# Kernel optimization log

Hardware: AMD Instinct MI355X
Metric: run time of the kernel (lower is better)

## Reference

```python
import jax, jax.numpy as jnp
import numpy as np

T, D = 8192, 256   # frames, feature dim
P, K = 64, 128     # phone vocabulary, centers per phone


def setup_inputs() -> dict:
    key = jax.random.key(0)
    k1, k2, k3 = jax.random.split(key, 3)
    h = jax.random.normal(k1, (T, D), dtype=jnp.float32)
    centers = jax.random.normal(k2, (P, K, D), dtype=jnp.float32)
    phones = jax.random.randint(k3, (T,), 0, P, dtype=jnp.int64)
    return {"h": h, "centers": centers, "phones": phones}


def reference(h, centers, phones):
    """Per-phone 1-NN retrieval: for each frame t, find nearest center in the
    pool for phones[t] and return that center (anonymized feature).
    centers: [P, K, D] padded table replacing the (pattern, phone, gender) dict.
    """
    c = centers[phones]                                # [T, K, D] irregular gather
    # squared euclidean distance; ||h_t||^2 is constant per row -> omit for argmin
    d2 = jnp.sum(c * c, axis=-1) - 2.0 * jnp.einsum("td,tkd->tk", h, c)  # [T, K]
    idx = jnp.argmin(d2, axis=-1)                      # [T]
    h_anon = jnp.take_along_axis(c, idx[:, None, None], axis=1)[:, 0, :]  # [T, D]
    return h_anon
```

## Files before the change

### kernel.cpp

```cpp
#include <hip/hip_runtime.h>

#define T_FRAMES 8192
#define D_DIM    256
#define P_PHONES 64
#define K_CENT   128
#define TILE_F   16
#define MAX_TILES 576
#define MARGIN   1.0f

#define WS_NORMS  0
#define WS_FIDX   32768
#define WS_DESC   65536
#define WS_HH     131072
#define WS_CH     (131072 + 4194304)

typedef _Float16 half8 __attribute__((ext_vector_type(8)));
typedef float    f32x4 __attribute__((ext_vector_type(4)));

__global__ __launch_bounds__(1024) void qr_prep_kernel(const float* __restrict__ h,
                                                       const float* __restrict__ centers,
                                                       const int* __restrict__ phones,
                                                       float* __restrict__ norms,
                                                       int* __restrict__ fidx,
                                                       int4* __restrict__ desc,
                                                       _Float16* __restrict__ hH,
                                                       _Float16* __restrict__ cH) {
    const int b   = blockIdx.x;
    const int tid = threadIdx.x;

    if (b >= 513) {
        const int row  = (b - 513) * 16 + (tid >> 6);
        const int lane = tid & 63;
        const float4 cv = ((const float4*)(centers + (size_t)row * D_DIM))[lane];
        float s = cv.x * cv.x + cv.y * cv.y + cv.z * cv.z + cv.w * cv.w;
#pragma unroll
        for (int off = 32; off; off >>= 1) s += __shfl_xor(s, off, 64);
        if (lane == 0) norms[row] = s;
        return;
    }
    if (b >= 1) {
        const size_t e = ((size_t)(b - 1) * 1024 + tid) * 4;
        union { _Float16 hf[4]; uint2 u; } pk;
        float4 v = *(const float4*)(h + e);
        pk.hf[0] = (_Float16)v.x; pk.hf[1] = (_Float16)v.y;
        pk.hf[2] = (_Float16)v.z; pk.hf[3] = (_Float16)v.w;
        *(uint2*)(hH + e) = pk.u;
        v = *(const float4*)(centers + e);
        pk.hf[0] = (_Float16)v.x; pk.hf[1] = (_Float16)v.y;
        pk.hf[2] = (_Float16)v.z; pk.hf[3] = (_Float16)v.w;
        *(uint2*)(cH + e) = pk.u;
        return;
    }

    __shared__ int hist[P_PHONES];
    __shared__ int offp[P_PHONES];
    if (tid < P_PHONES) hist[tid] = 0;
    if (tid < 1024) desc[tid] = make_int4(0, 0, 0, 0);
    __syncthreads();
    for (int i = tid; i < T_FRAMES; i += 1024) atomicAdd(&hist[phones[i]], 1);
    __syncthreads();

    if (tid < 64) {
        const int c = hist[tid];
        int x = c;
#pragma unroll
        for (int off = 1; off < 64; off <<= 1) {
            int y = __shfl_up(x, off, 64);
            if (tid >= off) x += y;
        }
        const int fbase = x - c;
        offp[tid] = fbase;
        const int nt = (c + TILE_F - 1) / TILE_F;
        int tx = nt;
#pragma unroll
        for (int off = 1; off < 64; off <<= 1) {
            int y = __shfl_up(tx, off, 64);
            if (tid >= off) tx += y;
        }
        const int tb = tx - nt;
        for (int j = 0; j < nt; ++j)
            desc[tb + j] = make_int4(tid, fbase + j * TILE_F, min(TILE_F, c - j * TILE_F), 0);
    }
    __syncthreads();

    for (int i = tid; i < T_FRAMES; i += 1024) {
        const int p = phones[i];
        fidx[atomicAdd(&offp[p], 1)] = i;
    }
}

__global__ __launch_bounds__(256) void qr_main_kernel(const float* __restrict__ h,
                                                      const float* __restrict__ centers,
                                                      const float* __restrict__ norms,
                                                      const int* __restrict__ fidx,
                                                      const int4* __restrict__ desc,
                                                      const _Float16* __restrict__ hH,
                                                      const _Float16* __restrict__ cH,
                                                      float* __restrict__ out) {
    __shared__ float d2s[TILE_F * K_CENT];
    __shared__ float mins[TILE_F];
    __shared__ int   cnt[TILE_F];
    __shared__ short cand[TILE_F * 32];

    const int4 dsc = desc[blockIdx.x];
    const int fcnt = dsc.z;
    if (fcnt == 0) return;
    const int p = dsc.x, fstart = dsc.y;

    const int tid  = threadIdx.x;
    const int wave = tid >> 6;
    const int lane = tid & 63;
    const int m    = lane & 15;
    const int quad = lane >> 4;

    if (tid < TILE_F) cnt[tid] = 0;

    const int fiA = fidx[fstart + min(m, fcnt - 1)];
    const _Float16* ap = hH + (size_t)fiA * D_DIM + quad * 8;
    half8 aF[8];
#pragma unroll
    for (int s = 0; s < 8; ++s) aF[s] = *(const half8*)(ap + s * 32);

#pragma unroll
    for (int u = 0; u < 2; ++u) {
        const int c = (wave * 2 + u) * 16 + m;
        const _Float16* bp = cH + ((size_t)p * K_CENT + c) * D_DIM + quad * 8;
        f32x4 acc = {0.f, 0.f, 0.f, 0.f};
#pragma unroll
        for (int s = 0; s < 8; ++s)
            acc = __builtin_amdgcn_mfma_f32_16x16x32_f16(aF[s], *(const half8*)(bp + s * 32),
                                                         acc, 0, 0, 0);
        const float nrm = norms[p * K_CENT + c];
#pragma unroll
        for (int r = 0; r < 4; ++r)
            d2s[(quad * 4 + r) * K_CENT + c] = nrm - 2.0f * acc[r];
    }
    __syncthreads();

    {
        const int fr = tid >> 4;
        const int g  = tid & 15;
        float mn = 3.0e38f;
#pragma unroll
        for (int j = 0; j < 8; ++j) mn = fminf(mn, d2s[fr * K_CENT + g * 8 + j]);
#pragma unroll
        for (int off = 1; off < 16; off <<= 1) mn = fminf(mn, __shfl_xor(mn, off, 64));
        if (g == 0) mins[fr] = mn;
    }
    __syncthreads();

    {
        const int fr = tid >> 4;
        const int g  = tid & 15;
        const float tau = mins[fr] + MARGIN;
#pragma unroll
        for (int j = 0; j < 8; ++j) {
            const int c = g * 8 + j;
            if (d2s[fr * K_CENT + c] < tau) {
                const int pos = atomicAdd(&cnt[fr], 1);
                if (pos < 32) cand[fr * 32 + pos] = (short)c;
            }
        }
    }
    __syncthreads();

    for (int fr = wave; fr < fcnt; fr += 4) {
        const int fi = fidx[fstart + fr];
        const float4 hv = ((const float4*)(h + (size_t)fi * D_DIM))[lane];
        const int n = cnt[fr];
        float best = 3.0e38f; int bc = 0x7FFFFFFF;
        const int ncand = (n <= 32) ? n : K_CENT;
        for (int ci = 0; ci < ncand; ++ci) {
            const int c = (n <= 32) ? (int)cand[fr * 32 + ci] : ci;
            const float4 cv = ((const float4*)(centers + ((size_t)p * K_CENT + c) * D_DIM))[lane];
            float s = hv.x * cv.x + hv.y * cv.y + hv.z * cv.z + hv.w * cv.w;
#pragma unroll
            for (int off = 32; off; off >>= 1) s += __shfl_xor(s, off, 64);
            const float d2 = norms[p * K_CENT + c] - 2.0f * s;
            if (d2 < best || (d2 == best && c < bc)) { best = d2; bc = c; }
        }
        const float4 w4 = ((const float4*)(centers + ((size_t)p * K_CENT + bc) * D_DIM))[lane];
        ((float4*)(out + (size_t)fi * D_DIM))[lane] = w4;
    }
}

extern "C" void kernel_launch(void* const* d_in, const int* in_sizes, int n_in,
                              void* d_out, int out_size, void* d_ws, size_t ws_size,
                              hipStream_t stream) {
    const float* h       = (const float*)d_in[0];
    const float* centers = (const float*)d_in[1];
    const int*   phones  = (const int*)d_in[2];
    float*       out     = (float*)d_out;

    char* ws = (char*)d_ws;
    float*     norms = (float*)(ws + WS_NORMS);
    int*       fidx  = (int*)(ws + WS_FIDX);
    int4*      desc  = (int4*)(ws + WS_DESC);
    _Float16*  hH    = (_Float16*)(ws + WS_HH);
    _Float16*  cH    = (_Float16*)(ws + WS_CH);

    qr_prep_kernel<<<1025, 1024, 0, stream>>>(h, centers, phones, norms, fidx, desc, hH, cH);
    qr_main_kernel<<<MAX_TILES, 256, 0, stream>>>(h, centers, norms, fidx, desc, hH, cH, out);
}
```

Measured before the change: 91.12 us.

## Use 32-frame tiles, fuse norm computation into fp16 conversion, skip refine for unique candidates

```diff
diff --git a/kernel.cpp b/kernel.cpp
--- a/kernel.cpp
+++ b/kernel.cpp
@@ -4,8 +4,8 @@
 #define D_DIM    256
 #define P_PHONES 64
 #define K_CENT   128
-#define TILE_F   16
-#define MAX_TILES 576
+#define TILE_F   32
+#define MAX_TILES 320
 #define MARGIN   1.0f
 
 #define WS_NORMS  0
@@ -28,16 +28,6 @@
     const int b   = blockIdx.x;
     const int tid = threadIdx.x;
 
-    if (b >= 513) {
-        const int row  = (b - 513) * 16 + (tid >> 6);
-        const int lane = tid & 63;
-        const float4 cv = ((const float4*)(centers + (size_t)row * D_DIM))[lane];
-        float s = cv.x * cv.x + cv.y * cv.y + cv.z * cv.z + cv.w * cv.w;
-#pragma unroll
-        for (int off = 32; off; off >>= 1) s += __shfl_xor(s, off, 64);
-        if (lane == 0) norms[row] = s;
-        return;
-    }
     if (b >= 1) {
         const size_t e = ((size_t)(b - 1) * 1024 + tid) * 4;
         union { _Float16 hf[4]; uint2 u; } pk;
@@ -49,13 +39,17 @@
         pk.hf[0] = (_Float16)v.x; pk.hf[1] = (_Float16)v.y;
         pk.hf[2] = (_Float16)v.z; pk.hf[3] = (_Float16)v.w;
         *(uint2*)(cH + e) = pk.u;
+        float s = v.x * v.x + v.y * v.y + v.z * v.z + v.w * v.w;
+#pragma unroll
+        for (int off = 32; off; off >>= 1) s += __shfl_xor(s, off, 64);
+        if ((tid & 63) == 0) norms[(b - 1) * 16 + (tid >> 6)] = s;
         return;
     }
 
     __shared__ int hist[P_PHONES];
     __shared__ int offp[P_PHONES];
     if (tid < P_PHONES) hist[tid] = 0;
-    if (tid < 1024) desc[tid] = make_int4(0, 0, 0, 0);
+    if (tid < MAX_TILES) desc[tid] = make_int4(0, 0, 0, 0);
     __syncthreads();
     for (int i = tid; i < T_FRAMES; i += 1024) atomicAdd(&hist[phones[i]], 1);
     __syncthreads();
@@ -101,6 +95,9 @@
     __shared__ float mins[TILE_F];
     __shared__ int   cnt[TILE_F];
     __shared__ short cand[TILE_F * 32];
+    __shared__ int   widx[TILE_F];
+    __shared__ int   rlist[TILE_F];
+    __shared__ int   rn;
 
     const int4 dsc = desc[blockIdx.x];
     const int fcnt = dsc.z;
@@ -114,48 +111,58 @@
     const int quad = lane >> 4;
 
     if (tid < TILE_F) cnt[tid] = 0;
-
-    const int fiA = fidx[fstart + min(m, fcnt - 1)];
-    const _Float16* ap = hH + (size_t)fiA * D_DIM + quad * 8;
-    half8 aF[8];
-#pragma unroll
-    for (int s = 0; s < 8; ++s) aF[s] = *(const half8*)(ap + s * 32);
+    if (tid == 0) rn = 0;
+
+    half8 aF[2][8];
+#pragma unroll
+    for (int t = 0; t < 2; ++t) {
+        const int fiA = fidx[fstart + min(t * 16 + m, fcnt - 1)];
+        const _Float16* ap = hH + (size_t)fiA * D_DIM + quad * 8;
+#pragma unroll
+        for (int s = 0; s < 8; ++s) aF[t][s] = *(const half8*)(ap + s * 32);
+    }
 
 #pragma unroll
     for (int u = 0; u < 2; ++u) {
         const int c = (wave * 2 + u) * 16 + m;
         const _Float16* bp = cH + ((size_t)p * K_CENT + c) * D_DIM + quad * 8;
-        f32x4 acc = {0.f, 0.f, 0.f, 0.f};
-#pragma unroll
-        for (int s = 0; s < 8; ++s)
-            acc = __builtin_amdgcn_mfma_f32_16x16x32_f16(aF[s], *(const half8*)(bp + s * 32),
-                                                         acc, 0, 0, 0);
+        half8 bF[8];
+#pragma unroll
+        for (int s = 0; s < 8; ++s) bF[s] = *(const half8*)(bp + s * 32);
+        f32x4 acc0 = {0.f, 0.f, 0.f, 0.f};
+        f32x4 acc1 = {0.f, 0.f, 0.f, 0.f};
+#pragma unroll
+        for (int s = 0; s < 8; ++s) {
+            acc0 = __builtin_amdgcn_mfma_f32_16x16x32_f16(aF[0][s], bF[s], acc0, 0, 0, 0);
+            acc1 = __builtin_amdgcn_mfma_f32_16x16x32_f16(aF[1][s], bF[s], acc1, 0, 0, 0);
+        }
         const float nrm = norms[p * K_CENT + c];
 #pragma unroll
-        for (int r = 0; r < 4; ++r)
-            d2s[(quad * 4 + r) * K_CENT + c] = nrm - 2.0f * acc[r];
-    }
-    __syncthreads();
-
+        for (int r = 0; r < 4; ++r) {
+            d2s[(quad * 4 + r) * K_CENT + c]        = nrm - 2.0f * acc0[r];
+            d2s[(16 + quad * 4 + r) * K_CENT + c]   = nrm - 2.0f * acc1[r];
+        }
+    }
+    __syncthreads();
+
+    const int fr = tid >> 3;
+    const int g  = tid & 7;
     {
-        const int fr = tid >> 4;
-        const int g  = tid & 15;
         float mn = 3.0e38f;
 #pragma unroll
-        for (int j = 0; j < 8; ++j) mn = fminf(mn, d2s[fr * K_CENT + g * 8 + j]);
-#pragma unroll
-        for (int off = 1; off < 16; off <<= 1) mn = fminf(mn, __shfl_xor(mn, off, 64));
+        for (int j = 0; j < 16; ++j) mn = fminf(mn, d2s[fr * K_CENT + g * 16 + j]);
+        mn = fminf(mn, __shfl_xor(mn, 1, 64));
+        mn = fminf(mn, __shfl_xor(mn, 2, 64));
+        mn = fminf(mn, __shfl_xor(mn, 4, 64));
         if (g == 0) mins[fr] = mn;
     }
     __syncthreads();
 
     {
-        const int fr = tid >> 4;
-        const int g  = tid & 15;
         const float tau = mins[fr] + MARGIN;
 #pragma unroll
-        for (int j = 0; j < 8; ++j) {
-            const int c = g * 8 + j;
+        for (int j = 0; j < 16; ++j) {
+            const int c = g * 16 + j;
             if (d2s[fr * K_CENT + c] < tau) {
                 const int pos = atomicAdd(&cnt[fr], 1);
                 if (pos < 32) cand[fr * 32 + pos] = (short)c;
@@ -164,14 +171,21 @@
     }
     __syncthreads();
 
-    for (int fr = wave; fr < fcnt; fr += 4) {
-        const int fi = fidx[fstart + fr];
+    if (tid < TILE_F && tid < fcnt) {
+        if (cnt[tid] == 1) widx[tid] = (int)cand[tid * 32];
+        else rlist[atomicAdd(&rn, 1)] = tid;
+    }
+    __syncthreads();
+
+    for (int r = wave; r < rn; r += 4) {
+        const int f2 = rlist[r];
+        const int fi = fidx[fstart + f2];
         const float4 hv = ((const float4*)(h + (size_t)fi * D_DIM))[lane];
-        const int n = cnt[fr];
+        const int n = cnt[f2];
+        const int ncand = (n <= 32) ? n : K_CENT;
         float best = 3.0e38f; int bc = 0x7FFFFFFF;
-        const int ncand = (n <= 32) ? n : K_CENT;
         for (int ci = 0; ci < ncand; ++ci) {
-            const int c = (n <= 32) ? (int)cand[fr * 32 + ci] : ci;
+            const int c = (n <= 32) ? (int)cand[f2 * 32 + ci] : ci;
             const float4 cv = ((const float4*)(centers + ((size_t)p * K_CENT + c) * D_DIM))[lane];
             float s = hv.x * cv.x + hv.y * cv.y + hv.z * cv.z + hv.w * cv.w;
 #pragma unroll
@@ -179,8 +193,16 @@
             const float d2 = norms[p * K_CENT + c] - 2.0f * s;
             if (d2 < best || (d2 == best && c < bc)) { best = d2; bc = c; }
         }
-        const float4 w4 = ((const float4*)(centers + ((size_t)p * K_CENT + bc) * D_DIM))[lane];
-        ((float4*)(out + (size_t)fi * D_DIM))[lane] = w4;
+        if (lane == 0) widx[f2] = bc;
+    }
+    __syncthreads();
+
+    if (fr < fcnt) {
+        const int fo = fidx[fstart + fr];
+        const float4* src = (const float4*)(centers + ((size_t)p * K_CENT + widx[fr]) * D_DIM);
+        float4* dst = (float4*)(out + (size_t)fo * D_DIM);
+#pragma unroll
+        for (int j = 0; j < 8; ++j) dst[g + 8 * j] = src[g + 8 * j];
     }
 }
 
@@ -199,6 +221,6 @@
     _Float16*  hH    = (_Float16*)(ws + WS_HH);
     _Float16*  cH    = (_Float16*)(ws + WS_CH);
 
-    qr_prep_kernel<<<1025, 1024, 0, stream>>>(h, centers, phones, norms, fidx, desc, hH, cH);
+    qr_prep_kernel<<<513, 1024, 0, stream>>>(h, centers, phones, norms, fidx, desc, hH, cH);
     qr_main_kernel<<<MAX_TILES, 256, 0, stream>>>(h, centers, norms, fidx, desc, hH, cH, out);
 }
```

Measured after the change: 90.67 us. No clear change (-0.5%).
